# Kernel tuning notes

Measured on AMD Instinct MI355X. Metric: run time of the kernel, lower is better.

## Reference

```python
import jax, jax.numpy as jnp
import numpy as np

B, S, D_IN, D_OUT = 4, 2048, 1024, 1024


def setup_inputs() -> dict:
    key = jax.random.key(0)
    k1, k2, k3, k4 = jax.random.split(key, 4)
    x = jax.random.normal(k1, (B, S, D_IN), dtype=jnp.float32)
    # torch nn.Linear weight layout: [d_out, d_in]
    wq = jax.random.normal(k2, (D_OUT, D_IN), dtype=jnp.float32) * (1.0 / np.sqrt(D_IN))
    wk = jax.random.normal(k3, (D_OUT, D_IN), dtype=jnp.float32) * (1.0 / np.sqrt(D_IN))
    wv = jax.random.normal(k4, (D_OUT, D_IN), dtype=jnp.float32) * (1.0 / np.sqrt(D_IN))
    return {"x": x, "wq": wq, "wk": wk, "wv": wv}


def reference(x, wq, wk, wv):
    # q,k,v: [b, s, d_out]
    q = jnp.einsum('bsd,od->bso', x, wq)
    k = jnp.einsum('bsd,od->bso', x, wk)
    v = jnp.einsum('bsd,od->bso', x, wv)
    scale = 1.0 / jnp.sqrt(jnp.asarray(k.shape[-1], dtype=q.dtype))
    scores = jnp.einsum('bqd,bkd->bqk', q, k)  # [b, s, s]
    s = scores.shape[-1]
    causal = jnp.tril(jnp.ones((s, s), dtype=bool))
    scores = jnp.where(causal, scores, -jnp.inf)
    attn = jax.nn.softmax(scores * scale, axis=-1)
    # dropout p=0.0 -> identity
    return jnp.einsum('bqk,bkd->bqd', attn, v)
```

## Files before the change

kernel.cpp:

```cpp
#include <hip/hip_runtime.h>
#include <hip/hip_bf16.h>
#include <cstdint>

#define BATCH 4
#define SEQ   2048
#define DIN   1024
#define DOUT  1024
#define SCALE 0.03125f

typedef unsigned short u16;
typedef float  f32x4  __attribute__((ext_vector_type(4)));
typedef __bf16 bf16x8 __attribute__((ext_vector_type(8)));

__device__ __forceinline__ u16 f2bf(float f) {
    unsigned u = __float_as_uint(f);
    unsigned r = 0x7fffu + ((u >> 16) & 1u);
    return (u16)((u + r) >> 16);
}

__device__ __forceinline__ f32x4 mfma16(bf16x8 a, bf16x8 b, f32x4 c) {
    return __builtin_amdgcn_mfma_f32_16x16x32_bf16(a, b, c, 0, 0, 0);
}

__device__ __forceinline__ void gl_lds16(const u16* g, u16* l) {
    __builtin_amdgcn_global_load_lds(
        (const __attribute__((address_space(1))) unsigned int*)g,
        (__attribute__((address_space(3))) unsigned int*)l, 16, 0, 0);
}

#define BAR    asm volatile("s_barrier" ::: "memory")
#define VMCNT3 asm volatile("s_waitcnt vmcnt(3)" ::: "memory")
#define VMCNT4 asm volatile("s_waitcnt vmcnt(4)" ::: "memory")
#define VMCNT0 asm volatile("s_waitcnt vmcnt(0)" ::: "memory")
#define LGKM0  asm volatile("s_waitcnt lgkmcnt(0)" ::: "memory")

__global__ __launch_bounds__(256) void cvt_all(const float* __restrict__ x,
                                               const float* __restrict__ wq,
                                               const float* __restrict__ wk,
                                               const float* __restrict__ wv,
                                               u16* __restrict__ dst,
                                               float* __restrict__ rowsum) {
    const size_t NX = (size_t)BATCH * SEQ * DIN;
    size_t gt = (size_t)blockIdx.x * 256 + threadIdx.x;
    if (gt < 1024) {
        f32x4 z = {0.f, 0.f, 0.f, 0.f};
        *(f32x4*)(rowsum + gt * 8) = z;
        *(f32x4*)(rowsum + gt * 8 + 4) = z;
    }
    size_t e = gt * 8;
    const float* src;
    size_t off;
    if (e < NX) { src = x; off = e; }
    else {
        size_t r = e - NX;
        int w = (int)(r >> 20);
        src = (w == 0) ? wq : (w == 1) ? wk : wv;
        off = r & ((1u << 20) - 1);
    }
    f32x4 a = *(const f32x4*)(src + off);
    f32x4 b = *(const f32x4*)(src + off + 4);
    uint4 o;
    o.x = (unsigned)f2bf(a[0]) | ((unsigned)f2bf(a[1]) << 16);
    o.y = (unsigned)f2bf(a[2]) | ((unsigned)f2bf(a[3]) << 16);
    o.z = (unsigned)f2bf(b[0]) | ((unsigned)f2bf(b[1]) << 16);
    o.w = (unsigned)f2bf(b[2]) | ((unsigned)f2bf(b[3]) << 16);
    *(uint4*)(dst + e) = o;
}

__device__ __forceinline__ void stg128(const u16* __restrict__ g, int ld,
                                       u16* unit, int tid) {
#pragma unroll
    for (int i = 0; i < 2; i++) {
        int D = (i * 512 + tid) * 16;
        int r = D >> 7, w = D & 127;
        int gcol = (w ^ ((r & 7) << 4)) >> 1;
        gl_lds16(g + (size_t)r * ld + gcol, unit + (i * 512 + (tid >> 6) * 64) * 8);
    }
}

__device__ __forceinline__ void stg192(const u16* __restrict__ g, int ld,
                                       u16* unit, int tid) {
#pragma unroll
    for (int i = 0; i < 3; i++) {
        int D = (i * 512 + tid) * 16;
        int r = D >> 7, w = D & 127;
        int gcol = (w ^ ((r & 7) << 4)) >> 1;
        gl_lds16(g + (size_t)r * ld + gcol, unit + (i * 512 + (tid >> 6) * 64) * 8);
    }
}

__device__ __forceinline__ void rd4(const u16* unit, int rowbase, int l15, int l4,
                                    bf16x8 f[4][2]) {
    const char* u = (const char*)unit;
#pragma unroll
    for (int i = 0; i < 4; i++) {
        int row = rowbase + i * 16 + l15;
#pragma unroll
        for (int kk = 0; kk < 2; kk++)
            f[i][kk] = *(const bf16x8*)(u + row * 128 +
                                        ((kk * 64 + l4 * 16) ^ ((row & 7) << 4)));
    }
}

__device__ __forceinline__ void rd3(const u16* unit, int rowbase, int l15, int l4,
                                    bf16x8 f[3][2]) {
    const char* u = (const char*)unit;
#pragma unroll
    for (int i = 0; i < 3; i++) {
        int row = rowbase + i * 16 + l15;
#pragma unroll
        for (int kk = 0; kk < 2; kk++)
            f[i][kk] = *(const bf16x8*)(u + row * 128 +
                                        ((kk * 64 + l4 * 16) ^ ((row & 7) << 4)));
    }
}

__device__ __forceinline__ void rd2k(const u16* unit, int row0, int l15, int l4,
                                     bf16x8 f[2]) {
    const char* u = (const char*)unit;
    int row = row0 + l15;
#pragma unroll
    for (int kk = 0; kk < 2; kk++)
        f[kk] = *(const bf16x8*)(u + row * 128 +
                                 ((kk * 64 + l4 * 16) ^ ((row & 7) << 4)));
}

__device__ __forceinline__ void g64_body(u16* lds, const u16* __restrict__ Ag,
                                         int lda, const u16* __restrict__ Bg,
                                         int ldb, int nkt, int wm, int wn,
                                         int l15, int l4, int tid,
                                         f32x4 acc[4][2]) {
    bf16x8 a[4][2], b0[2], b1[2];
    u16* A0 = lds;          u16* B0 = lds + 8192;
    u16* A1 = lds + 16384;  u16* B1 = lds + 24576;
    stg128(Ag, lda, A0, tid);      stg128(Bg, ldb, B0, tid);
    stg128(Ag + 64, lda, A1, tid); stg128(Bg + 64, ldb, B1, tid);
    VMCNT4; BAR;
    for (int t = 0; t < nkt; t += 2) {
        {
            const int k2 = ((t + 2 < nkt) ? t + 2 : nkt - 1) * 64;
            rd4(A0, wm * 64, l15, l4, a);
            rd2k(B0, wn * 32, l15, l4, b0);
            rd2k(B0, wn * 32 + 16, l15, l4, b1);
            BAR;
            __builtin_amdgcn_s_setprio(1);
#pragma unroll
            for (int kk = 0; kk < 2; kk++)
#pragma unroll
                for (int mi = 0; mi < 4; mi++)
                    acc[mi][0] = mfma16(a[mi][kk], b0[kk], acc[mi][0]);
            __builtin_amdgcn_s_setprio(0);
            LGKM0; BAR;
            stg128(Ag + k2, lda, A0, tid);
            stg128(Bg + k2, ldb, B0, tid);
            VMCNT4; BAR;
            __builtin_amdgcn_s_setprio(1);
#pragma unroll
            for (int kk = 0; kk < 2; kk++)
#pragma unroll
                for (int mi = 0; mi < 4; mi++)
                    acc[mi][1] = mfma16(a[mi][kk], b1[kk], acc[mi][1]);
            __builtin_amdgcn_s_setprio(0);
            BAR;
        }
        {
            const int k3 = ((t + 3 < nkt) ? t + 3 : nkt - 1) * 64;
            rd4(A1, wm * 64, l15, l4, a);
            rd2k(B1, wn * 32, l15, l4, b0);
            rd2k(B1, wn * 32 + 16, l15, l4, b1);
            BAR;
            __builtin_amdgcn_s_setprio(1);
#pragma unroll
            for (int kk = 0; kk < 2; kk++)
#pragma unroll
                for (int mi = 0; mi < 4; mi++)
                    acc[mi][0] = mfma16(a[mi][kk], b0[kk], acc[mi][0]);
            __builtin_amdgcn_s_setprio(0);
            LGKM0; BAR;
            stg128(Ag + k3, lda, A1, tid);
            stg128(Bg + k3, ldb, B1, tid);
            VMCNT4; BAR;
            __builtin_amdgcn_s_setprio(1);
#pragma unroll
            for (int kk = 0; kk < 2; kk++)
#pragma unroll
                for (int mi = 0; mi < 4; mi++)
                    acc[mi][1] = mfma16(a[mi][kk], b1[kk], acc[mi][1]);
            __builtin_amdgcn_s_setprio(0);
            BAR;
        }
    }
    VMCNT0;
}

#define QKV_PH0(AU, BU, ANX0, ANX1, K1)                                      \
    rd4((AU), 0, l15, l4, a);                                                \
    rd3((BU), wn * 48, l15, l4, b);                                          \
    stg128(Ag + (K1), DIN, (ANX0), tid);                                     \
    stg128(Ag + (size_t)128 * DIN + (K1), DIN, (ANX1), tid);                 \
    BAR;                                                                     \
    __builtin_amdgcn_s_setprio(1);                                           \
    _Pragma("unroll") for (int kk = 0; kk < 2; kk++)                         \
    _Pragma("unroll") for (int mi = 0; mi < 4; mi++)                         \
    _Pragma("unroll") for (int ni = 0; ni < 3; ni++)                         \
        acc[mi][ni] = mfma16(a[mi][kk], b[ni][kk], acc[mi][ni]);             \
    __builtin_amdgcn_s_setprio(0);                                           \
    BAR;

#define QKV_PH1(AU, BCUR, K2)                                                \
    rd4((AU), 64, l15, l4, a);                                               \
    stg192(Bg + (K2), DIN, (BCUR), tid);                                     \
    VMCNT3; BAR;                                                             \
    __builtin_amdgcn_s_setprio(1);                                           \
    _Pragma("unroll") for (int kk = 0; kk < 2; kk++)                         \
    _Pragma("unroll") for (int mi = 0; mi < 4; mi++)                         \
    _Pragma("unroll") for (int ni = 0; ni < 3; ni++)                         \
        acc[4 + mi][ni] = mfma16(a[mi][kk], b[ni][kk], acc[4 + mi][ni]);     \
    __builtin_amdgcn_s_setprio(0);                                           \
    BAR;

__global__ __launch_bounds__(512) void qkv_gemm192(const u16* __restrict__ xb,
                                                   const u16* __restrict__ wb,
                                                   u16* __restrict__ qkv,
                                                   u16* __restrict__ vt) {
    extern __shared__ __align__(16) u16 lds[];
    const int tid = threadIdx.x, lane = tid & 63, wid = tid >> 6;
    const int wm = wid >> 2, wn = wid & 3;
    const int l15 = lane & 15, l4 = lane >> 4;

    u16* A00 = lds;          u16* A01 = lds + 8192;
    u16* A10 = lds + 16384;  u16* A11 = lds + 24576;
    u16* B0  = lds + 32768;  u16* B1  = lds + 45056;
    u16* Ar0 = lds + wm * 8192;
    u16* Ar1 = lds + 16384 + wm * 8192;

    for (int tile = blockIdx.x; tile < 512; tile += 256) {
        const int wg = (tile & 7) * 64 + (tile >> 3);
        const int mt = wg & 31, nt = wg >> 5;
        const int m0 = mt * 256, n0 = nt * 192;
        const u16* Ag = xb + (size_t)m0 * DIN;
        const u16* Bg = wb + (size_t)n0 * DIN;
        f32x4 acc[8][3] = {};
        bf16x8 a[4][2], b[3][2];

        stg128(Ag, DIN, A00, tid);
        stg128(Ag + (size_t)128 * DIN, DIN, A01, tid);
        stg192(Bg, DIN, B0, tid);
        stg192(Bg + 64, DIN, B1, tid);
        VMCNT3;
        BAR;

        for (int i = 0; i < 8; i++) {
            const int k1 = (2 * i + 1) * 64;
            const int k2 = ((2 * i + 2 < 16) ? 2 * i + 2 : 15) * 64;
            const int k3 = ((2 * i + 3 < 16) ? 2 * i + 3 : 15) * 64;
            QKV_PH0(Ar0, B0, A10, A11, k1)
            QKV_PH1(Ar0, B0, k2)
            QKV_PH0(Ar1, B1, A00, A01, k2)
            QKV_PH1(Ar1, B1, k3)
        }
        VMCNT0;

#pragma unroll
        for (int ai = 0; ai < 8; ai++)
#pragma unroll
            for (int bj = 0; bj < 3; bj++) {
                const int colb = n0 + wn * 48 + bj * 16;
                const int row = m0 + wm * 128 + ai * 16 + l4 * 4;
                if (colb >= 2 * DOUT) {
                    int d = colb + l15 - 2 * DOUT;
                    int batch = row >> 11, s0 = row & 2047;
                    uint2 o;
                    o.x = (unsigned)f2bf(acc[ai][bj][0]) |
                          ((unsigned)f2bf(acc[ai][bj][1]) << 16);
                    o.y = (unsigned)f2bf(acc[ai][bj][2]) |
                          ((unsigned)f2bf(acc[ai][bj][3]) << 16);
                    *(uint2*)&vt[(size_t)batch * DOUT * SEQ + (size_t)d * SEQ + s0] = o;
                } else {
                    const int wsel = colb >> 10;
                    u16* Op = qkv + (size_t)wsel * ((size_t)BATCH * SEQ * DOUT);
                    const int col = (colb & 1023) + l15;
#pragma unroll
                    for (int rr = 0; rr < 4; rr++)
                        Op[(size_t)(row + rr) * DOUT + col] = f2bf(acc[ai][bj][rr]);
                }
            }
    }
}

__global__ __launch_bounds__(512, 4) void qk_g64(const u16* __restrict__ qg,
                                                 const u16* __restrict__ kg,
                                                 u16* __restrict__ sg,
                                                 float* __restrict__ rowsum) {
    extern __shared__ __align__(16) u16 lds[];
    const int bxx = blockIdx.x, batch = blockIdx.y;
    int mt = 0, base = 0;
#pragma unroll 16
    for (int m = 0; m < 16; m++) {
        int c = m + 1;
        if (bxx < base + c) { mt = m; break; }
        base += c;
    }
    const int nt = bxx - base;
    const int m0 = mt * 128, n0 = nt * 128;
    const int tid = threadIdx.x, lane = tid & 63;
    const int wm = (tid >> 6) >> 2, wn = (tid >> 6) & 3;
    const int l15 = lane & 15, l4 = lane >> 4;
    const size_t bo = (size_t)batch * SEQ * DOUT;

    f32x4 acc[4][2] = {};
    g64_body(lds, qg + bo + (size_t)m0 * DOUT, DOUT,
             kg + bo + (size_t)n0 * DOUT, DOUT, 16,
             wm, wn, l15, l4, tid, acc);

    u16* Sp = sg + (size_t)batch * SEQ * SEQ;
    float* Rs = rowsum + (size_t)batch * SEQ;
#pragma unroll
    for (int ai = 0; ai < 4; ai++)
#pragma unroll
        for (int rr = 0; rr < 4; rr++) {
            int q = m0 + wm * 64 + ai * 16 + l4 * 4 + rr;
            float rp = 0.f;
#pragma unroll
            for (int bj = 0; bj < 2; bj++) {
                int kc = n0 + wn * 32 + bj * 16 + l15;
                float p = (kc <= q) ? __expf(acc[ai][bj][rr] * SCALE) : 0.f;
                rp += p;
                Sp[(size_t)q * SEQ + kc] = f2bf(p);
            }
#pragma unroll
            for (int off = 8; off >= 1; off >>= 1) rp += __shfl_xor(rp, off, 16);
            if (l15 == 0) atomicAdd(&Rs[q], rp);
        }
}

__global__ __launch_bounds__(512, 4) void pv_g64(const u16* __restrict__ pg,
                                                 const u16* __restrict__ vtg,
                                                 const float* __restrict__ rowsum,
                                                 float* __restrict__ og) {
    extern __shared__ __align__(16) u16 lds[];
    const int mt = 15 - (int)blockIdx.x;
    const int n0 = blockIdx.y * 128, batch = blockIdx.z;
    const int m0 = mt * 128;
    const int nkt = (mt + 1) * 2;
    const int tid = threadIdx.x, lane = tid & 63;
    const int wm = (tid >> 6) >> 2, wn = (tid >> 6) & 3;
    const int l15 = lane & 15, l4 = lane >> 4;
    const u16* Pb = pg + (size_t)batch * SEQ * SEQ;
    const u16* Vb = vtg + (size_t)batch * DOUT * SEQ + (size_t)n0 * SEQ;
    const float* Rs = rowsum + (size_t)batch * SEQ;
    float* Ob = og + (size_t)batch * SEQ * DOUT;

    f32x4 acc[4][2] = {};
    g64_body(lds, Pb + (size_t)m0 * SEQ, SEQ, Vb, SEQ, nkt,
             wm, wn, l15, l4, tid, acc);

#pragma unroll
    for (int ai = 0; ai < 4; ai++)
#pragma unroll
        for (int rr = 0; rr < 4; rr++) {
            int q = m0 + wm * 64 + ai * 16 + l4 * 4 + rr;
            float inv = 1.0f / Rs[q];
#pragma unroll
            for (int bj = 0; bj < 2; bj++) {
                int d = n0 + wn * 32 + bj * 16 + l15;
                Ob[(size_t)q * DOUT + d] = acc[ai][bj][rr] * inv;
            }
        }
}

extern "C" void kernel_launch(void* const* d_in, const int* in_sizes, int n_in,
                              void* d_out, int out_size, void* d_ws, size_t ws_size,
                              hipStream_t stream) {
    const float* x  = (const float*)d_in[0];
    const float* wq = (const float*)d_in[1];
    const float* wk = (const float*)d_in[2];
    const float* wv = (const float*)d_in[3];
    float* out = (float*)d_out;

    const size_t NX  = (size_t)BATCH * SEQ * DIN;
    const size_t NWT = (size_t)DOUT * DIN;
    u16* xb  = (u16*)d_ws;
    u16* wb  = xb + NX;
    u16* qkv = wb + 3 * NWT;
    u16* vt  = qkv + 3 * NX;
    u16* sb  = vt + NX;
    float* rowsum = (float*)(sb + (size_t)BATCH * SEQ * SEQ);

    cvt_all<<<(NX + 3 * NWT) / 8 / 256, 256, 0, stream>>>(x, wq, wk, wv, xb, rowsum);

    (void)hipFuncSetAttribute((const void*)qkv_gemm192,
                              hipFuncAttributeMaxDynamicSharedMemorySize, 114688);
    (void)hipFuncSetAttribute((const void*)qk_g64,
                              hipFuncAttributeMaxDynamicSharedMemorySize, 65536);
    (void)hipFuncSetAttribute((const void*)pv_g64,
                              hipFuncAttributeMaxDynamicSharedMemorySize, 65536);

    qkv_gemm192<<<dim3(256), dim3(512), 114688, stream>>>(xb, wb, qkv, vt);

    qk_g64<<<dim3(136, BATCH), dim3(512), 65536, stream>>>(qkv, qkv + NX, sb, rowsum);

    pv_g64<<<dim3(16, 8, 4), dim3(512), 65536, stream>>>(sb, vt, rowsum, out);
}
```

Baseline: 158.5 us.

## Use 4-wave 64x64 warp tiles for QK and PV GEMMs

Changes the QK and PV kernels from 8 waves of 64x32 tiles to 4 waves of 64x64 tiles per 128x128 block. Each wave now reads more B fragments per A fragment, which cuts LDS reads per MFMA, but each thread issues twice as many global-to-LDS loads and holds twice as many accumulators. The PV kernel also reverses the tile order for batches 2-3 so that long and short causal tiles are interleaved across the grid for load balance. Fewer waves per block lowers latency hiding, and the higher register use may reduce occupancy.

Result: faster. 147.6 us (median of 3 runs) (-6.9%).

```diff
diff --git a/kernel.cpp b/kernel.cpp
--- a/kernel.cpp
+++ b/kernel.cpp
@@ -30,7 +30,7 @@
 
 #define BAR    asm volatile("s_barrier" ::: "memory")
 #define VMCNT3 asm volatile("s_waitcnt vmcnt(3)" ::: "memory")
-#define VMCNT4 asm volatile("s_waitcnt vmcnt(4)" ::: "memory")
+#define VMCNT8 asm volatile("s_waitcnt vmcnt(8)" ::: "memory")
 #define VMCNT0 asm volatile("s_waitcnt vmcnt(0)" ::: "memory")
 #define LGKM0  asm volatile("s_waitcnt lgkmcnt(0)" ::: "memory")
 
@@ -89,6 +89,17 @@
     }
 }
 
+__device__ __forceinline__ void stg4(const u16* __restrict__ g, int ld,
+                                     u16* unit, int tid) {
+#pragma unroll
+    for (int i = 0; i < 4; i++) {
+        int D = (i * 256 + tid) * 16;
+        int r = D >> 7, w = D & 127;
+        int gcol = (w ^ ((r & 7) << 4)) >> 1;
+        gl_lds16(g + (size_t)r * ld + gcol, unit + (i * 256 + (tid >> 6) * 64) * 8);
+    }
+}
+
 __device__ __forceinline__ void rd4(const u16* unit, int rowbase, int l15, int l4,
                                     bf16x8 f[4][2]) {
     const char* u = (const char*)unit;
@@ -115,77 +126,73 @@
     }
 }
 
-__device__ __forceinline__ void rd2k(const u16* unit, int row0, int l15, int l4,
-                                     bf16x8 f[2]) {
-    const char* u = (const char*)unit;
-    int row = row0 + l15;
-#pragma unroll
-    for (int kk = 0; kk < 2; kk++)
-        f[kk] = *(const bf16x8*)(u + row * 128 +
-                                 ((kk * 64 + l4 * 16) ^ ((row & 7) << 4)));
-}
-
-__device__ __forceinline__ void g64_body(u16* lds, const u16* __restrict__ Ag,
-                                         int lda, const u16* __restrict__ Bg,
-                                         int ldb, int nkt, int wm, int wn,
-                                         int l15, int l4, int tid,
-                                         f32x4 acc[4][2]) {
-    bf16x8 a[4][2], b0[2], b1[2];
+__device__ __forceinline__ void g4_body(u16* lds, const u16* __restrict__ Ag,
+                                        int lda, const u16* __restrict__ Bg,
+                                        int ldb, int nkt, int wm, int wn,
+                                        int l15, int l4, int tid,
+                                        f32x4 acc[4][4]) {
+    bf16x8 a[4][2], b[4][2];
     u16* A0 = lds;          u16* B0 = lds + 8192;
     u16* A1 = lds + 16384;  u16* B1 = lds + 24576;
-    stg128(Ag, lda, A0, tid);      stg128(Bg, ldb, B0, tid);
-    stg128(Ag + 64, lda, A1, tid); stg128(Bg + 64, ldb, B1, tid);
-    VMCNT4; BAR;
+    stg4(Ag, lda, A0, tid);      stg4(Bg, ldb, B0, tid);
+    stg4(Ag + 64, lda, A1, tid); stg4(Bg + 64, ldb, B1, tid);
+    VMCNT8; BAR;
     for (int t = 0; t < nkt; t += 2) {
         {
             const int k2 = ((t + 2 < nkt) ? t + 2 : nkt - 1) * 64;
             rd4(A0, wm * 64, l15, l4, a);
-            rd2k(B0, wn * 32, l15, l4, b0);
-            rd2k(B0, wn * 32 + 16, l15, l4, b1);
+            rd4(B0, wn * 64, l15, l4, b);
             BAR;
             __builtin_amdgcn_s_setprio(1);
 #pragma unroll
             for (int kk = 0; kk < 2; kk++)
 #pragma unroll
                 for (int mi = 0; mi < 4; mi++)
-                    acc[mi][0] = mfma16(a[mi][kk], b0[kk], acc[mi][0]);
+#pragma unroll
+                    for (int ni = 0; ni < 2; ni++)
+                        acc[mi][ni] = mfma16(a[mi][kk], b[ni][kk], acc[mi][ni]);
             __builtin_amdgcn_s_setprio(0);
             LGKM0; BAR;
-            stg128(Ag + k2, lda, A0, tid);
-            stg128(Bg + k2, ldb, B0, tid);
-            VMCNT4; BAR;
+            stg4(Ag + k2, lda, A0, tid);
+            stg4(Bg + k2, ldb, B0, tid);
+            VMCNT8; BAR;
             __builtin_amdgcn_s_setprio(1);
 #pragma unroll
             for (int kk = 0; kk < 2; kk++)
 #pragma unroll
                 for (int mi = 0; mi < 4; mi++)
-                    acc[mi][1] = mfma16(a[mi][kk], b1[kk], acc[mi][1]);
+#pragma unroll
+                    for (int ni = 2; ni < 4; ni++)
+                        acc[mi][ni] = mfma16(a[mi][kk], b[ni][kk], acc[mi][ni]);
             __builtin_amdgcn_s_setprio(0);
             BAR;
         }
         {
             const int k3 = ((t + 3 < nkt) ? t + 3 : nkt - 1) * 64;
             rd4(A1, wm * 64, l15, l4, a);
-            rd2k(B1, wn * 32, l15, l4, b0);
-            rd2k(B1, wn * 32 + 16, l15, l4, b1);
+            rd4(B1, wn * 64, l15, l4, b);
             BAR;
             __builtin_amdgcn_s_setprio(1);
 #pragma unroll
             for (int kk = 0; kk < 2; kk++)
 #pragma unroll
                 for (int mi = 0; mi < 4; mi++)
-                    acc[mi][0] = mfma16(a[mi][kk], b0[kk], acc[mi][0]);
+#pragma unroll
+                    for (int ni = 0; ni < 2; ni++)
+                        acc[mi][ni] = mfma16(a[mi][kk], b[ni][kk], acc[mi][ni]);
             __builtin_amdgcn_s_setprio(0);
             LGKM0; BAR;
-            stg128(Ag + k3, lda, A1, tid);
-            stg128(Bg + k3, ldb, B1, tid);
-            VMCNT4; BAR;
+            stg4(Ag + k3, lda, A1, tid);
+            stg4(Bg + k3, ldb, B1, tid);
+            VMCNT8; BAR;
             __builtin_amdgcn_s_setprio(1);
 #pragma unroll
             for (int kk = 0; kk < 2; kk++)
 #pragma unroll
                 for (int mi = 0; mi < 4; mi++)
-                    acc[mi][1] = mfma16(a[mi][kk], b1[kk], acc[mi][1]);
+#pragma unroll
+                    for (int ni = 2; ni < 4; ni++)
+                        acc[mi][ni] = mfma16(a[mi][kk], b[ni][kk], acc[mi][ni]);
             __builtin_amdgcn_s_setprio(0);
             BAR;
         }
@@ -288,10 +295,10 @@
     }
 }
 
-__global__ __launch_bounds__(512, 4) void qk_g64(const u16* __restrict__ qg,
-                                                 const u16* __restrict__ kg,
-                                                 u16* __restrict__ sg,
-                                                 float* __restrict__ rowsum) {
+__global__ __launch_bounds__(256) void qk4(const u16* __restrict__ qg,
+                                           const u16* __restrict__ kg,
+                                           u16* __restrict__ sg,
+                                           float* __restrict__ rowsum) {
     extern __shared__ __align__(16) u16 lds[];
     const int bxx = blockIdx.x, batch = blockIdx.y;
     int mt = 0, base = 0;
@@ -303,15 +310,15 @@
     }
     const int nt = bxx - base;
     const int m0 = mt * 128, n0 = nt * 128;
-    const int tid = threadIdx.x, lane = tid & 63;
-    const int wm = (tid >> 6) >> 2, wn = (tid >> 6) & 3;
+    const int tid = threadIdx.x, lane = tid & 63, wid = tid >> 6;
+    const int wm = wid >> 1, wn = wid & 1;
     const int l15 = lane & 15, l4 = lane >> 4;
     const size_t bo = (size_t)batch * SEQ * DOUT;
 
-    f32x4 acc[4][2] = {};
-    g64_body(lds, qg + bo + (size_t)m0 * DOUT, DOUT,
-             kg + bo + (size_t)n0 * DOUT, DOUT, 16,
-             wm, wn, l15, l4, tid, acc);
+    f32x4 acc[4][4] = {};
+    g4_body(lds, qg + bo + (size_t)m0 * DOUT, DOUT,
+            kg + bo + (size_t)n0 * DOUT, DOUT, 16,
+            wm, wn, l15, l4, tid, acc);
 
     u16* Sp = sg + (size_t)batch * SEQ * SEQ;
     float* Rs = rowsum + (size_t)batch * SEQ;
@@ -322,8 +329,8 @@
             int q = m0 + wm * 64 + ai * 16 + l4 * 4 + rr;
             float rp = 0.f;
 #pragma unroll
-            for (int bj = 0; bj < 2; bj++) {
-                int kc = n0 + wn * 32 + bj * 16 + l15;
+            for (int bj = 0; bj < 4; bj++) {
+                int kc = n0 + wn * 64 + bj * 16 + l15;
                 float p = (kc <= q) ? __expf(acc[ai][bj][rr] * SCALE) : 0.f;
                 rp += p;
                 Sp[(size_t)q * SEQ + kc] = f2bf(p);
@@ -334,26 +341,26 @@
         }
 }
 
-__global__ __launch_bounds__(512, 4) void pv_g64(const u16* __restrict__ pg,
-                                                 const u16* __restrict__ vtg,
-                                                 const float* __restrict__ rowsum,
-                                                 float* __restrict__ og) {
+__global__ __launch_bounds__(256) void pv4(const u16* __restrict__ pg,
+                                           const u16* __restrict__ vtg,
+                                           const float* __restrict__ rowsum,
+                                           float* __restrict__ og) {
     extern __shared__ __align__(16) u16 lds[];
-    const int mt = 15 - (int)blockIdx.x;
+    const int mt = (blockIdx.z < 2) ? (15 - (int)blockIdx.x) : (int)blockIdx.x;
     const int n0 = blockIdx.y * 128, batch = blockIdx.z;
     const int m0 = mt * 128;
     const int nkt = (mt + 1) * 2;
-    const int tid = threadIdx.x, lane = tid & 63;
-    const int wm = (tid >> 6) >> 2, wn = (tid >> 6) & 3;
+    const int tid = threadIdx.x, lane = tid & 63, wid = tid >> 6;
+    const int wm = wid >> 1, wn = wid & 1;
     const int l15 = lane & 15, l4 = lane >> 4;
     const u16* Pb = pg + (size_t)batch * SEQ * SEQ;
     const u16* Vb = vtg + (size_t)batch * DOUT * SEQ + (size_t)n0 * SEQ;
     const float* Rs = rowsum + (size_t)batch * SEQ;
     float* Ob = og + (size_t)batch * SEQ * DOUT;
 
-    f32x4 acc[4][2] = {};
-    g64_body(lds, Pb + (size_t)m0 * SEQ, SEQ, Vb, SEQ, nkt,
-             wm, wn, l15, l4, tid, acc);
+    f32x4 acc[4][4] = {};
+    g4_body(lds, Pb + (size_t)m0 * SEQ, SEQ, Vb, SEQ, nkt,
+            wm, wn, l15, l4, tid, acc);
 
 #pragma unroll
     for (int ai = 0; ai < 4; ai++)
@@ -362,8 +369,8 @@
             int q = m0 + wm * 64 + ai * 16 + l4 * 4 + rr;
             float inv = 1.0f / Rs[q];
 #pragma unroll
-            for (int bj = 0; bj < 2; bj++) {
-                int d = n0 + wn * 32 + bj * 16 + l15;
+            for (int bj = 0; bj < 4; bj++) {
+                int d = n0 + wn * 64 + bj * 16 + l15;
                 Ob[(size_t)q * DOUT + d] = acc[ai][bj][rr] * inv;
             }
         }
@@ -391,14 +398,14 @@
 
     (void)hipFuncSetAttribute((const void*)qkv_gemm192,
                               hipFuncAttributeMaxDynamicSharedMemorySize, 114688);
-    (void)hipFuncSetAttribute((const void*)qk_g64,
+    (void)hipFuncSetAttribute((const void*)qk4,
                               hipFuncAttributeMaxDynamicSharedMemorySize, 65536);
-    (void)hipFuncSetAttribute((const void*)pv_g64,
+    (void)hipFuncSetAttribute((const void*)pv4,
                               hipFuncAttributeMaxDynamicSharedMemorySize, 65536);
 
     qkv_gemm192<<<dim3(256), dim3(512), 114688, stream>>>(xb, wb, qkv, vt);
 
-    qk_g64<<<dim3(136, BATCH), dim3(512), 65536, stream>>>(qkv, qkv + NX, sb, rowsum);
-
-    pv_g64<<<dim3(16, 8, 4), dim3(512), 65536, stream>>>(sb, vt, rowsum, out);
-}
+    qk4<<<dim3(136, BATCH), dim3(256), 65536, stream>>>(qkv, qkv + NX, sb, rowsum);
+
+    pv4<<<dim3(16, 8, 4), dim3(256), 65536, stream>>>(sb, vt, rowsum, out);
+}
```
